# Kernel tuning notes

Hardware: AMD Instinct MI355X
Metric: run time of the kernel (lower is better)

Reference implementation:

```python
import jax, jax.numpy as jnp
import numpy as np

T = 20
DT = 0.001
TAU = 0.02
V_TH = 0.5
V_RESET = 0.0


def setup_inputs() -> dict:
    key = jax.random.key(0)
    ks = jax.random.split(key, 5)
    batch, embed_dim, expert_dim, num_experts, hidden_dim = 256, 1024, 64, 16, 1024
    return {
        "query_embedding": jax.random.normal(ks[0], (batch, embed_dim), dtype=jnp.float32),
        "gate_bias": jax.random.normal(ks[1], (num_experts,), dtype=jnp.float32),
        "temperature": jnp.ones((1,), dtype=jnp.float32),
        "W_in": jax.random.normal(ks[2], (embed_dim, expert_dim), dtype=jnp.float32) * 0.03,
        "experts": jax.random.normal(ks[3], (num_experts, expert_dim, hidden_dim), dtype=jnp.float32) * 0.1,
        "gate_kernel": jax.random.normal(ks[4], (expert_dim, num_experts), dtype=jnp.float32) * 0.1,
    }


def reference(query_embedding, gate_bias, temperature, W_in, experts, gate_kernel):
    dtype = query_embedding.dtype
    x = (query_embedding @ W_in).astype(dtype)  # [B, D]

    # Poisson encoding: Bernoulli spikes with rate sigmoid(x), fixed module key.
    rates = jax.nn.sigmoid(x)
    _, bern_key = jax.random.split(jax.random.key(0))
    input_spikes = jax.random.bernoulli(bern_key, rates, shape=(T,) + rates.shape).astype(dtype)  # [T, B, D]

    # Softmax MoE gate (computed in fp32 as in original).
    gate_logits = x @ gate_kernel + gate_bias[None, :].astype(dtype)  # [B, E]
    gate_probs = jax.nn.softmax(
        gate_logits.astype(jnp.float32) / temperature.astype(jnp.float32), axis=-1
    ).astype(dtype)

    E, _, H = experts.shape
    B = x.shape[0]
    leak = DT / TAU

    def time_step(v, s_t):
        # v: [E, B, H]; s_t: [B, D]
        current = jnp.einsum('bd,edh->ebh', s_t, experts)
        new_v = v + (current - v) * leak
        spike = (new_v >= V_TH).astype(dtype)
        new_v = new_v * (1.0 - spike) + V_RESET * spike
        return new_v, spike

    v0 = jnp.zeros((E, B, H), dtype=dtype)
    _, spikes_all = jax.lax.scan(time_step, v0, input_spikes)  # [T, E, B, H]

    avg_spikes = jnp.mean(spikes_all, axis=0)  # [E, B, H]
    # Gate-weighted combine over experts -> [B, H]
    return jnp.einsum('ebh,be->bh', avg_spikes, gate_probs)
```

## Files before the change

kernel.cpp:

```cpp
#include <hip/hip_runtime.h>

typedef unsigned int u32;
typedef unsigned short u16;
typedef unsigned char u8;
typedef __attribute__((ext_vector_type(8))) short bf16x8;
typedef __attribute__((ext_vector_type(4))) float f32x4;

#define JAX_PARTITIONABLE 1
#define FLAG_DELTA 5e-4f
#define FLAG_CAP 262144u

__host__ __device__ static inline void tf2x32(u32 k0, u32 k1, u32 x0, u32 x1,
                                              u32* o0, u32* o1)
{
  const u32 ks2 = k0 ^ k1 ^ 0x1BD11BDAu;
#define TF_R(v, r) (((v) << (r)) | ((v) >> (32 - (r))))
#define TF_RND(r) do { x0 += x1; x1 = TF_R(x1, r); x1 ^= x0; } while (0);
  x0 += k0; x1 += k1;
  TF_RND(13) TF_RND(15) TF_RND(26) TF_RND(6)
  x0 += k1;  x1 += ks2 + 1u;
  TF_RND(17) TF_RND(29) TF_RND(16) TF_RND(24)
  x0 += ks2; x1 += k0 + 2u;
  TF_RND(13) TF_RND(15) TF_RND(26) TF_RND(6)
  x0 += k0;  x1 += k1 + 3u;
  TF_RND(17) TF_RND(29) TF_RND(16) TF_RND(24)
  x0 += k1;  x1 += ks2 + 4u;
  TF_RND(13) TF_RND(15) TF_RND(26) TF_RND(6)
  x0 += ks2; x1 += k0 + 5u;
  *o0 = x0; *o1 = x1;
#undef TF_RND
#undef TF_R
}

__device__ static inline u16 f2bf(float f) {
  u32 u = __float_as_uint(f);
  return (u16)((u + 0x7FFFu + ((u >> 16) & 1u)) >> 16);
}
__device__ static inline float bf2f(u16 b) {
  return __uint_as_float(((u32)b) << 16);
}

__global__ __launch_bounds__(64) void k_gate(
    const float* __restrict__ q, const float* __restrict__ win,
    const float* __restrict__ gbias, const float* __restrict__ temp,
    const float* __restrict__ gk, float* __restrict__ rates,
    float* __restrict__ gateo, u32* __restrict__ fcnt)
{
  const int b = blockIdx.x, j = threadIdx.x;
  if (b == 0 && j == 0) fcnt[0] = 0;
  __shared__ float qs[1024];
  __shared__ float xs[64];
  const float* __restrict__ qr = q + b * 1024;
  for (int d = j; d < 1024; d += 64) qs[d] = qr[d];
  __syncthreads();

  const float* __restrict__ wc = win + j;
  float bufA[64], bufB[64];
#pragma unroll
  for (int i = 0; i < 64; ++i) bufA[i] = wc[i * 64];
  float c = 0.f;
#pragma unroll
  for (int ch = 0; ch < 8; ++ch) {
#pragma unroll
    for (int i = 0; i < 64; ++i)
      bufB[i] = wc[((2 * ch + 1) * 64 + i) * 64];
#pragma unroll
    for (int i = 0; i < 64; ++i)
      c = __builtin_fmaf(qs[2 * ch * 64 + i], bufA[i], c);
    if (ch < 7) {
#pragma unroll
      for (int i = 0; i < 64; ++i)
        bufA[i] = wc[((2 * ch + 2) * 64 + i) * 64];
    }
#pragma unroll
    for (int i = 0; i < 64; ++i)
      c = __builtin_fmaf(qs[(2 * ch + 1) * 64 + i], bufB[i], c);
  }
  const float x = c;
  float r;
  if (x >= 0.f) r = __fdiv_rn(1.f, __fadd_rn(1.f, expf(-x)));
  else { const float ex = expf(x); r = __fdiv_rn(ex, __fadd_rn(1.f, ex)); }
  rates[b * 64 + j] = r;
  xs[j] = x;
  __syncthreads();
  if (j < 16) {
    float l = 0.f;
    for (int d = 0; d < 64; ++d)
      l = __builtin_fmaf(xs[d], gk[d * 16 + j], l);
    l = __fadd_rn(l, gbias[j]);
    l = __fdiv_rn(l, temp[0]);
    float m = l;
    for (int off = 1; off < 16; off <<= 1) m = fmaxf(m, __shfl_xor(m, off, 16));
    const float p = expf(__fsub_rn(l, m));
    float s = p;
    for (int off = 1; off < 16; off <<= 1) s += __shfl_xor(s, off, 16);
    gateo[b * 16 + j] = __fdiv_rn(p, s);
  }
}

__global__ __launch_bounds__(256) void k_prep(
    const float* __restrict__ ex, u16* __restrict__ wsp, float* __restrict__ ext,
    const float* __restrict__ rates, u16* __restrict__ spk, u32 bk0, u32 bk1)
{
  if (blockIdx.x < 256) {
    const int e = blockIdx.x >> 4, hb = blockIdx.x & 15;
    const int tl = threadIdx.x & 63, tg = threadIdx.x >> 6;
    __shared__ float tile[64][65];
#pragma unroll
    for (int r = 0; r < 16; ++r) {
      const int d = r * 4 + tg;
      tile[d][tl] = ex[((size_t)e * 64 + d) * 1024 + hb * 64 + tl];
    }
    __syncthreads();
#pragma unroll
    for (int r = 0; r < 16; ++r) {
      const int hl = r * 4 + tg;
      const float wraw = tile[tl][hl];
      const float wv = wraw * 0.05f;
      const u16 hi = f2bf(wv);
      const u16 lo = f2bf(wv - bf2f(hi));
      const size_t o = ((size_t)e * 1024 + hb * 64 + hl) * 64 + tl;
      wsp[o] = hi;
      wsp[o + 1048576] = lo;
      ext[o] = wraw;
    }
  } else {
    const u32 g = (blockIdx.x - 256) * 256u + threadIdx.x;
#if JAX_PARTITIONABLE
    u32 o0, o1;
    tf2x32(bk0, bk1, 0u, g, &o0, &o1);
    const u32 bits = o0 ^ o1;
    const float r = rates[g & 16383u];
    const float u = __uint_as_float((bits >> 9) | 0x3f800000u) - 1.0f;
    spk[g] = (u < r) ? (u16)0x3F80 : (u16)0;
#else
    u32 o0, o1;
    tf2x32(bk0, bk1, g, g + 163840u, &o0, &o1);
    const float r = rates[g & 16383u];
    const float ua = __uint_as_float((o0 >> 9) | 0x3f800000u) - 1.0f;
    const float ub = __uint_as_float((o1 >> 9) | 0x3f800000u) - 1.0f;
    spk[g] = (ua < r) ? (u16)0x3F80 : (u16)0;
    spk[g + 163840u] = (ub < r) ? (u16)0x3F80 : (u16)0;
#endif
  }
}

__global__ __launch_bounds__(256, 3) void k_lif(
    const u16* __restrict__ spk, const u16* __restrict__ wsp,
    u8* __restrict__ cnt, u32* __restrict__ fcnt, u32* __restrict__ flist)
{
  const int hblk = blockIdx.x, bblk = blockIdx.y, e = blockIdx.z;
  const int tid = threadIdx.x;
  const int w = tid >> 6, lane = tid & 63;
  const int wb = w & 1, wh = w >> 1;
  const int lr = lane & 15, lg = lane >> 4;
  const int b0 = bblk * 32 + wb * 16;
  const int h0 = hblk * 128 + wh * 64;

  bf16x8 bf[4][2][2];
#pragma unroll
  for (int nt = 0; nt < 4; ++nt)
#pragma unroll
    for (int kc = 0; kc < 2; ++kc)
#pragma unroll
      for (int s = 0; s < 2; ++s)
        bf[nt][kc][s] = *(const bf16x8*)(wsp +
            ((size_t)((s * 16 + e) * 1024 + h0 + nt * 16 + lr)) * 64 + kc * 32 + lg * 8);
#pragma unroll
  for (int nt = 0; nt < 4; ++nt)
#pragma unroll
    for (int kc = 0; kc < 2; ++kc)
#pragma unroll
      for (int s = 0; s < 2; ++s)
        asm volatile("" : "+v"(bf[nt][kc][s]));

  f32x4 v[4];
  int cn[4][4];
  u32 fl = 0;
#pragma unroll
  for (int nt = 0; nt < 4; ++nt) {
    v[nt] = (f32x4){0.f, 0.f, 0.f, 0.f};
#pragma unroll
    for (int i = 0; i < 4; ++i) cn[nt][i] = 0;
  }

  const u16* abase = spk + (size_t)(b0 + lr) * 64 + lg * 8;
  bf16x8 a0 = *(const bf16x8*)(abase);
  bf16x8 a1 = *(const bf16x8*)(abase + 32);

#define PROC(VAL, CREF, BIT) {                                  \
    const float tt = (VAL) - 0.5f;                              \
    if (__builtin_fabsf(tt) < FLAG_DELTA) fl |= (1u << (BIT));  \
    const bool sp = (tt >= 0.f);                                \
    (CREF) += sp;                                               \
    (VAL) = sp ? 0.f : (VAL); }

  for (int t = 0; t < 20; ++t) {
    const int tn = (t < 19) ? t + 1 : 19;
    const bf16x8 n0 = *(const bf16x8*)(abase + (size_t)tn * 16384);
    const bf16x8 n1 = *(const bf16x8*)(abase + (size_t)tn * 16384 + 32);
#pragma unroll
    for (int nt = 0; nt < 4; ++nt) {
      f32x4 accA = v[nt] * 0.95f;
      accA = __builtin_amdgcn_mfma_f32_16x16x32_bf16(a0, bf[nt][0][0], accA, 0, 0, 0);
      accA = __builtin_amdgcn_mfma_f32_16x16x32_bf16(a1, bf[nt][1][0], accA, 0, 0, 0);
      f32x4 accB = (f32x4){0.f, 0.f, 0.f, 0.f};
      accB = __builtin_amdgcn_mfma_f32_16x16x32_bf16(a0, bf[nt][0][1], accB, 0, 0, 0);
      accB = __builtin_amdgcn_mfma_f32_16x16x32_bf16(a1, bf[nt][1][1], accB, 0, 0, 0);
      f32x4 nv = accA + accB;
      PROC(nv.x, cn[nt][0], nt * 4 + 0)
      PROC(nv.y, cn[nt][1], nt * 4 + 1)
      PROC(nv.z, cn[nt][2], nt * 4 + 2)
      PROC(nv.w, cn[nt][3], nt * 4 + 3)
      v[nt] = nv;
    }
    a0 = n0; a1 = n1;
  }
#undef PROC

#pragma unroll
  for (int nt = 0; nt < 4; ++nt) {
    const int h = h0 + nt * 16 + lr;
#pragma unroll
    for (int i = 0; i < 4; ++i) {
      const int b = b0 + lg * 4 + i;
      cnt[((size_t)e * 256 + b) * 1024 + h] = (u8)cn[nt][i];
    }
  }

  const u32 myc = (u32)__builtin_popcount((int)fl);
  u32 pre = myc;
#pragma unroll
  for (int off = 1; off < 64; off <<= 1) {
    const u32 xx = __shfl_up(pre, off, 64);
    if (lane >= off) pre += xx;
  }
  const u32 tot = __shfl(pre, 63, 64);
  if (tot) {
    u32 base = 0;
    if (lane == 63) base = atomicAdd(fcnt, tot);
    base = __shfl(base, 63, 64);
    u32 slot = base + pre - myc;
    if (fl) {
#pragma unroll
      for (int nt = 0; nt < 4; ++nt)
#pragma unroll
        for (int i = 0; i < 4; ++i)
          if ((fl >> (nt * 4 + i)) & 1u) {
            if (slot < FLAG_CAP)
              flist[slot] = ((u32)e << 18) | ((u32)(b0 + lg * 4 + i) << 10) |
                            (u32)(h0 + nt * 16 + lr);
            slot++;
          }
    }
  }
}

__global__ __launch_bounds__(256) void k_fix(
    const u16* __restrict__ spk, const float* __restrict__ ext,
    const u32* __restrict__ fcnt, const u32* __restrict__ flist,
    u8* __restrict__ cnt)
{
  u32 n = fcnt[0];
  if (n > FLAG_CAP) n = FLAG_CAP;
  for (u32 i = blockIdx.x * 256u + threadIdx.x; i < n; i += 65536u) {
    const u32 p = flist[i];
    const int h = (int)(p & 1023u), b = (int)((p >> 10) & 255u), e = (int)(p >> 18);
    const float* __restrict__ wbp = ext + ((size_t)e * 1024 + h) * 64;
    float wr[64];
#pragma unroll
    for (int d = 0; d < 64; ++d) wr[d] = wbp[d];
    float v = 0.f;
    int c = 0;
    for (int t = 0; t < 20; ++t) {
      const uint4* __restrict__ sr = (const uint4*)(spk + (size_t)(t * 256 + b) * 64);
      float cc = 0.f;
#pragma unroll
      for (int w8 = 0; w8 < 8; ++w8) {
        const uint4 sv = sr[w8];
        cc = __builtin_fmaf(__uint_as_float(sv.x << 16),         wr[w8 * 8 + 0], cc);
        cc = __builtin_fmaf(__uint_as_float(sv.x & 0xFFFF0000u), wr[w8 * 8 + 1], cc);
        cc = __builtin_fmaf(__uint_as_float(sv.y << 16),         wr[w8 * 8 + 2], cc);
        cc = __builtin_fmaf(__uint_as_float(sv.y & 0xFFFF0000u), wr[w8 * 8 + 3], cc);
        cc = __builtin_fmaf(__uint_as_float(sv.z << 16),         wr[w8 * 8 + 4], cc);
        cc = __builtin_fmaf(__uint_as_float(sv.z & 0xFFFF0000u), wr[w8 * 8 + 5], cc);
        cc = __builtin_fmaf(__uint_as_float(sv.w << 16),         wr[w8 * 8 + 6], cc);
        cc = __builtin_fmaf(__uint_as_float(sv.w & 0xFFFF0000u), wr[w8 * 8 + 7], cc);
      }
      const float nv = __fadd_rn(v, __fmul_rn(__fsub_rn(cc, v), 0.05f));
      if (nv >= 0.5f) { c++; v = 0.f; } else v = nv;
    }
    cnt[((size_t)e * 256 + b) * 1024 + h] = (u8)c;
  }
}

__global__ __launch_bounds__(256) void k_combine(
    const u8* __restrict__ cnt, const float* __restrict__ gateo,
    float* __restrict__ out)
{
  const int idx = blockIdx.x * 256 + threadIdx.x;
  const int b = idx >> 10, h = idx & 1023;
  float s = 0.f;
#pragma unroll
  for (int e = 0; e < 16; ++e) {
    const float av = __fdiv_rn((float)cnt[((size_t)e * 256 + b) * 1024 + h], 20.f);
    s = __builtin_fmaf(av, gateo[b * 16 + e], s);
  }
  out[idx] = s;
}

extern "C" void kernel_launch(void* const* d_in, const int* in_sizes, int n_in,
                              void* d_out, int out_size, void* d_ws, size_t ws_size,
                              hipStream_t stream)
{
  (void)in_sizes; (void)n_in; (void)out_size; (void)ws_size;
  const float* q     = (const float*)d_in[0];
  const float* gbias = (const float*)d_in[1];
  const float* temp  = (const float*)d_in[2];
  const float* win   = (const float*)d_in[3];
  const float* ex    = (const float*)d_in[4];
  const float* gk    = (const float*)d_in[5];
  float* out = (float*)d_out;

  char* ws = (char*)d_ws;
  u16*  spk   = (u16*)(ws + 0);
  float* rates = (float*)(ws + 655360);
  float* gateo = (float*)(ws + 720896);
  u16*  wsp   = (u16*)(ws + 737280);
  u8*   cnt   = (u8*)(ws + 4931584);
  u32*  fcnt  = (u32*)(ws + 9125888);
  u32*  flist = (u32*)(ws + 9126912);
  float* ext  = (float*)(ws + 10175488);

  u32 bk0, bk1;
#if JAX_PARTITIONABLE
  tf2x32(0u, 0u, 0u, 1u, &bk0, &bk1);
#else
  u32 a0o, a1o, b0o, b1o;
  tf2x32(0u, 0u, 0u, 2u, &a0o, &a1o);
  tf2x32(0u, 0u, 1u, 3u, &b0o, &b1o);
  bk0 = a1o; bk1 = b1o;
#endif

  k_gate<<<256, 64, 0, stream>>>(q, win, gbias, temp, gk, rates, gateo, fcnt);
#if JAX_PARTITIONABLE
  k_prep<<<256 + 1280, 256, 0, stream>>>(ex, wsp, ext, rates, spk, bk0, bk1);
#else
  k_prep<<<256 + 640, 256, 0, stream>>>(ex, wsp, ext, rates, spk, bk0, bk1);
#endif
  k_lif<<<dim3(8, 8, 16), 256, 0, stream>>>(spk, wsp, cnt, fcnt, flist);
  k_fix<<<256, 256, 0, stream>>>(spk, ext, fcnt, flist, cnt);
  k_combine<<<1024, 256, 0, stream>>>(cnt, gateo, out);
}
```

Baseline: 166.7 us.

## Retile LIF kernel to smaller H tiles, batch gate rows, vectorize combine and fix

```diff
diff --git a/kernel.cpp b/kernel.cpp
--- a/kernel.cpp
+++ b/kernel.cpp
@@ -40,20 +40,25 @@
   return __uint_as_float(((u32)b) << 16);
 }
 
-__global__ __launch_bounds__(64) void k_gate(
+__global__ __launch_bounds__(256) void k_gate(
     const float* __restrict__ q, const float* __restrict__ win,
     const float* __restrict__ gbias, const float* __restrict__ temp,
     const float* __restrict__ gk, float* __restrict__ rates,
     float* __restrict__ gateo, u32* __restrict__ fcnt)
 {
-  const int b = blockIdx.x, j = threadIdx.x;
-  if (b == 0 && j == 0) fcnt[0] = 0;
-  __shared__ float qs[1024];
-  __shared__ float xs[64];
-  const float* __restrict__ qr = q + b * 1024;
-  for (int d = j; d < 1024; d += 64) qs[d] = qr[d];
+  const int tid = threadIdx.x;
+  if (blockIdx.x == 0 && tid == 0) fcnt[0] = 0;
+  __shared__ float qs[4][1024];
+  const int b4 = blockIdx.x * 4;
+#pragma unroll
+  for (int r = 0; r < 4; ++r) {
+    const float4 qv = *(const float4*)(q + (size_t)(b4 + r) * 1024 + tid * 4);
+    *(float4*)(&qs[r][tid * 4]) = qv;
+  }
   __syncthreads();
 
+  const int w = tid >> 6, j = tid & 63;
+  const int b = b4 + w;
   const float* __restrict__ wc = win + j;
   float bufA[64], bufB[64];
 #pragma unroll
@@ -66,7 +71,7 @@
       bufB[i] = wc[((2 * ch + 1) * 64 + i) * 64];
 #pragma unroll
     for (int i = 0; i < 64; ++i)
-      c = __builtin_fmaf(qs[2 * ch * 64 + i], bufA[i], c);
+      c = __builtin_fmaf(qs[w][2 * ch * 64 + i], bufA[i], c);
     if (ch < 7) {
 #pragma unroll
       for (int i = 0; i < 64; ++i)
@@ -74,28 +79,28 @@
     }
 #pragma unroll
     for (int i = 0; i < 64; ++i)
-      c = __builtin_fmaf(qs[(2 * ch + 1) * 64 + i], bufB[i], c);
+      c = __builtin_fmaf(qs[w][(2 * ch + 1) * 64 + i], bufB[i], c);
   }
   const float x = c;
   float r;
   if (x >= 0.f) r = __fdiv_rn(1.f, __fadd_rn(1.f, expf(-x)));
   else { const float ex = expf(x); r = __fdiv_rn(ex, __fadd_rn(1.f, ex)); }
   rates[b * 64 + j] = r;
-  xs[j] = x;
-  __syncthreads();
-  if (j < 16) {
-    float l = 0.f;
-    for (int d = 0; d < 64; ++d)
-      l = __builtin_fmaf(xs[d], gk[d * 16 + j], l);
-    l = __fadd_rn(l, gbias[j]);
-    l = __fdiv_rn(l, temp[0]);
-    float m = l;
-    for (int off = 1; off < 16; off <<= 1) m = fmaxf(m, __shfl_xor(m, off, 16));
-    const float p = expf(__fsub_rn(l, m));
-    float s = p;
-    for (int off = 1; off < 16; off <<= 1) s += __shfl_xor(s, off, 16);
-    gateo[b * 16 + j] = __fdiv_rn(p, s);
-  }
+
+  const int jj = j & 15;
+  float l = 0.f;
+  for (int dd = 0; dd < 64; ++dd) {
+    const float xv = __shfl(x, dd, 64);
+    l = __builtin_fmaf(xv, gk[dd * 16 + jj], l);
+  }
+  l = __fadd_rn(l, gbias[jj]);
+  l = __fdiv_rn(l, temp[0]);
+  float m = l;
+  for (int off = 1; off < 16; off <<= 1) m = fmaxf(m, __shfl_xor(m, off, 16));
+  const float p = expf(__fsub_rn(l, m));
+  float s = p;
+  for (int off = 1; off < 16; off <<= 1) s += __shfl_xor(s, off, 16);
+  if (j < 16) gateo[b * 16 + j] = __fdiv_rn(p, s);
 }
 
 __global__ __launch_bounds__(256) void k_prep(
@@ -145,7 +150,7 @@
   }
 }
 
-__global__ __launch_bounds__(256, 3) void k_lif(
+__global__ __launch_bounds__(256) void k_lif(
     const u16* __restrict__ spk, const u16* __restrict__ wsp,
     u8* __restrict__ cnt, u32* __restrict__ fcnt, u32* __restrict__ flist)
 {
@@ -155,34 +160,26 @@
   const int wb = w & 1, wh = w >> 1;
   const int lr = lane & 15, lg = lane >> 4;
   const int b0 = bblk * 32 + wb * 16;
-  const int h0 = hblk * 128 + wh * 64;
-
-  bf16x8 bf[4][2][2];
-#pragma unroll
-  for (int nt = 0; nt < 4; ++nt)
-#pragma unroll
-    for (int kc = 0; kc < 2; ++kc)
-#pragma unroll
-      for (int s = 0; s < 2; ++s)
-        bf[nt][kc][s] = *(const bf16x8*)(wsp +
-            ((size_t)((s * 16 + e) * 1024 + h0 + nt * 16 + lr)) * 64 + kc * 32 + lg * 8);
-#pragma unroll
-  for (int nt = 0; nt < 4; ++nt)
-#pragma unroll
-    for (int kc = 0; kc < 2; ++kc)
-#pragma unroll
-      for (int s = 0; s < 2; ++s)
-        asm volatile("" : "+v"(bf[nt][kc][s]));
-
-  f32x4 v[4];
-  int cn[4][4];
+  const int h0 = hblk * 64 + wh * 32;
+
+#define FRAG(NT, KC, S) (*(const bf16x8*)(wsp + \
+    ((size_t)((S) * 16 + e) * 1024 + h0 + (NT) * 16 + lr) * 64 + (KC) * 32 + lg * 8))
+  bf16x8 bh00 = FRAG(0, 0, 0), bh01 = FRAG(0, 1, 0);
+  bf16x8 bh10 = FRAG(1, 0, 0), bh11 = FRAG(1, 1, 0);
+  bf16x8 bl00 = FRAG(0, 0, 1), bl01 = FRAG(0, 1, 1);
+  bf16x8 bl10 = FRAG(1, 0, 1), bl11 = FRAG(1, 1, 1);
+#undef FRAG
+  asm volatile("" : "+v"(bh00), "+v"(bh01), "+v"(bh10), "+v"(bh11));
+  asm volatile("" : "+v"(bl00), "+v"(bl01), "+v"(bl10), "+v"(bl11));
+
+  f32x4 v0 = (f32x4){0.f, 0.f, 0.f, 0.f};
+  f32x4 v1 = (f32x4){0.f, 0.f, 0.f, 0.f};
+  int cn[2][4];
+#pragma unroll
+  for (int nt = 0; nt < 2; ++nt)
+#pragma unroll
+    for (int i = 0; i < 4; ++i) cn[nt][i] = 0;
   u32 fl = 0;
-#pragma unroll
-  for (int nt = 0; nt < 4; ++nt) {
-    v[nt] = (f32x4){0.f, 0.f, 0.f, 0.f};
-#pragma unroll
-    for (int i = 0; i < 4; ++i) cn[nt][i] = 0;
-  }
 
   const u16* abase = spk + (size_t)(b0 + lr) * 64 + lg * 8;
   bf16x8 a0 = *(const bf16x8*)(abase);
@@ -199,27 +196,40 @@
     const int tn = (t < 19) ? t + 1 : 19;
     const bf16x8 n0 = *(const bf16x8*)(abase + (size_t)tn * 16384);
     const bf16x8 n1 = *(const bf16x8*)(abase + (size_t)tn * 16384 + 32);
-#pragma unroll
-    for (int nt = 0; nt < 4; ++nt) {
-      f32x4 accA = v[nt] * 0.95f;
-      accA = __builtin_amdgcn_mfma_f32_16x16x32_bf16(a0, bf[nt][0][0], accA, 0, 0, 0);
-      accA = __builtin_amdgcn_mfma_f32_16x16x32_bf16(a1, bf[nt][1][0], accA, 0, 0, 0);
+    {
+      f32x4 accA = v0 * 0.95f;
+      accA = __builtin_amdgcn_mfma_f32_16x16x32_bf16(a0, bh00, accA, 0, 0, 0);
+      accA = __builtin_amdgcn_mfma_f32_16x16x32_bf16(a1, bh01, accA, 0, 0, 0);
       f32x4 accB = (f32x4){0.f, 0.f, 0.f, 0.f};
-      accB = __builtin_amdgcn_mfma_f32_16x16x32_bf16(a0, bf[nt][0][1], accB, 0, 0, 0);
-      accB = __builtin_amdgcn_mfma_f32_16x16x32_bf16(a1, bf[nt][1][1], accB, 0, 0, 0);
+      accB = __builtin_amdgcn_mfma_f32_16x16x32_bf16(a0, bl00, accB, 0, 0, 0);
+      accB = __builtin_amdgcn_mfma_f32_16x16x32_bf16(a1, bl01, accB, 0, 0, 0);
       f32x4 nv = accA + accB;
-      PROC(nv.x, cn[nt][0], nt * 4 + 0)
-      PROC(nv.y, cn[nt][1], nt * 4 + 1)
-      PROC(nv.z, cn[nt][2], nt * 4 + 2)
-      PROC(nv.w, cn[nt][3], nt * 4 + 3)
-      v[nt] = nv;
+      PROC(nv.x, cn[0][0], 0)
+      PROC(nv.y, cn[0][1], 1)
+      PROC(nv.z, cn[0][2], 2)
+      PROC(nv.w, cn[0][3], 3)
+      v0 = nv;
+    }
+    {
+      f32x4 accA = v1 * 0.95f;
+      accA = __builtin_amdgcn_mfma_f32_16x16x32_bf16(a0, bh10, accA, 0, 0, 0);
+      accA = __builtin_amdgcn_mfma_f32_16x16x32_bf16(a1, bh11, accA, 0, 0, 0);
+      f32x4 accB = (f32x4){0.f, 0.f, 0.f, 0.f};
+      accB = __builtin_amdgcn_mfma_f32_16x16x32_bf16(a0, bl10, accB, 0, 0, 0);
+      accB = __builtin_amdgcn_mfma_f32_16x16x32_bf16(a1, bl11, accB, 0, 0, 0);
+      f32x4 nv = accA + accB;
+      PROC(nv.x, cn[1][0], 4)
+      PROC(nv.y, cn[1][1], 5)
+      PROC(nv.z, cn[1][2], 6)
+      PROC(nv.w, cn[1][3], 7)
+      v1 = nv;
     }
     a0 = n0; a1 = n1;
   }
 #undef PROC
 
 #pragma unroll
-  for (int nt = 0; nt < 4; ++nt) {
+  for (int nt = 0; nt < 2; ++nt) {
     const int h = h0 + nt * 16 + lr;
 #pragma unroll
     for (int i = 0; i < 4; ++i) {
@@ -243,7 +253,7 @@
     u32 slot = base + pre - myc;
     if (fl) {
 #pragma unroll
-      for (int nt = 0; nt < 4; ++nt)
+      for (int nt = 0; nt < 2; ++nt)
 #pragma unroll
         for (int i = 0; i < 4; ++i)
           if ((fl >> (nt * 4 + i)) & 1u) {
@@ -269,7 +279,11 @@
     const float* __restrict__ wbp = ext + ((size_t)e * 1024 + h) * 64;
     float wr[64];
 #pragma unroll
-    for (int d = 0; d < 64; ++d) wr[d] = wbp[d];
+    for (int d4 = 0; d4 < 16; ++d4) {
+      const float4 wv = *(const float4*)(wbp + d4 * 4);
+      wr[d4 * 4 + 0] = wv.x; wr[d4 * 4 + 1] = wv.y;
+      wr[d4 * 4 + 2] = wv.z; wr[d4 * 4 + 3] = wv.w;
+    }
     float v = 0.f;
     int c = 0;
     for (int t = 0; t < 20; ++t) {
@@ -299,14 +313,21 @@
     float* __restrict__ out)
 {
   const int idx = blockIdx.x * 256 + threadIdx.x;
-  const int b = idx >> 10, h = idx & 1023;
-  float s = 0.f;
+  const int b = idx >> 8, hq = idx & 255;
+  const int h0 = hq * 4;
+  float s0 = 0.f, s1 = 0.f, s2 = 0.f, s3 = 0.f;
 #pragma unroll
   for (int e = 0; e < 16; ++e) {
-    const float av = __fdiv_rn((float)cnt[((size_t)e * 256 + b) * 1024 + h], 20.f);
-    s = __builtin_fmaf(av, gateo[b * 16 + e], s);
-  }
-  out[idx] = s;
+    const uchar4 cv = *(const uchar4*)(cnt + ((size_t)e * 256 + b) * 1024 + h0);
+    const float g = gateo[b * 16 + e];
+    s0 = __builtin_fmaf(__fdiv_rn((float)cv.x, 20.f), g, s0);
+    s1 = __builtin_fmaf(__fdiv_rn((float)cv.y, 20.f), g, s1);
+    s2 = __builtin_fmaf(__fdiv_rn((float)cv.z, 20.f), g, s2);
+    s3 = __builtin_fmaf(__fdiv_rn((float)cv.w, 20.f), g, s3);
+  }
+  float4 o;
+  o.x = s0; o.y = s1; o.z = s2; o.w = s3;
+  *(float4*)(out + (size_t)b * 1024 + h0) = o;
 }
 
 extern "C" void kernel_launch(void* const* d_in, const int* in_sizes, int n_in,
@@ -342,13 +363,13 @@
   bk0 = a1o; bk1 = b1o;
 #endif
 
-  k_gate<<<256, 64, 0, stream>>>(q, win, gbias, temp, gk, rates, gateo, fcnt);
+  k_gate<<<64, 256, 0, stream>>>(q, win, gbias, temp, gk, rates, gateo, fcnt);
 #if JAX_PARTITIONABLE
   k_prep<<<256 + 1280, 256, 0, stream>>>(ex, wsp, ext, rates, spk, bk0, bk1);
 #else
   k_prep<<<256 + 640, 256, 0, stream>>>(ex, wsp, ext, rates, spk, bk0, bk1);
 #endif
-  k_lif<<<dim3(8, 8, 16), 256, 0, stream>>>(spk, wsp, cnt, fcnt, flist);
+  k_lif<<<dim3(16, 8, 16), 256, 0, stream>>>(spk, wsp, cnt, fcnt, flist);
   k_fix<<<256, 256, 0, stream>>>(spk, ext, fcnt, flist, cnt);
-  k_combine<<<1024, 256, 0, stream>>>(cnt, gateo, out);
-}
+  k_combine<<<256, 256, 0, stream>>>(cnt, gateo, out);
+}
```

Result: slower. 195.7 us (+17.3%).
